# Optimization experiments

Measured on AMD Instinct MI355X. Metric: run time of the kernel, lower is better.

## Reference

```python
import jax, jax.numpy as jnp
import numpy as np

N_WAY = 5
K_SHOT = 1
QUERY = 75          # queries per class -> 375 total
PRJ = 14            # projections per support class
C, H, W = 512, 10, 10
NUM_NODE = H * W
SINK_EPS = 0.05     # entropic regularization (on max-normalized cost)
SINK_ITERS = 50


def setup_inputs() -> dict:
    key = jax.random.key(0)
    k1, k2 = jax.random.split(key)
    n_support = N_WAY * K_SHOT * PRJ
    num_query = N_WAY * QUERY
    feat = jax.random.normal(k1, (n_support + num_query, C, H, W), dtype=jnp.float32)
    label = jax.random.randint(k2, (num_query,), 0, N_WAY)
    return {"feat": feat, "label": label}


def _sinkhorn(cost, r, c, eps=SINK_EPS, iters=SINK_ITERS):
    """Batched entropic OT (log-domain Sinkhorn), replacing the per-pair
    cv2.EMD CPU solve. cost: [..., n, m]; r: [..., n]; c: [..., m].
    r and c each sum to NUM_NODE, so total transported mass is NUM_NODE,
    matching the cv2.EMD flow scale. Scaling the cost by a positive scalar
    does not change the (exact-)OT plan, so we max-normalize per pair for a
    consistent effective regularization."""
    scale = jnp.max(cost, axis=(-1, -2), keepdims=True) + 1e-6
    cost = cost / scale
    log_r = jnp.log(r)
    log_c = jnp.log(c)

    def body(fg, _):
        f, g = fg
        f = eps * (log_r - jax.nn.logsumexp((g[..., None, :] - cost) / eps, axis=-1))
        g = eps * (log_c - jax.nn.logsumexp((f[..., :, None] - cost) / eps, axis=-2))
        return (f, g), None

    init = (jnp.zeros_like(r), jnp.zeros_like(c))
    (f, g), _ = jax.lax.scan(body, init, None, length=iters)
    return jnp.exp((f[..., :, None] + g[..., None, :] - cost) / eps)


def reference(feat, label):
    n_support = N_WAY * K_SHOT * PRJ
    support = feat[:n_support].reshape(N_WAY, PRJ, C, H, W)
    query = feat[n_support:]                       # [nq, C, H, W]
    proto = support.mean(axis=1)                   # [way, C, H, W]
    nq = query.shape[0]

    # --- get_weight_vector: <A_node_feat, global_avg(B)> per (A,B) pair ---
    proto_avg = proto.mean(axis=(2, 3))            # [way, C]
    query_avg = query.mean(axis=(2, 3))            # [nq, C]
    qf = query.reshape(nq, C, NUM_NODE)
    pf = proto.reshape(N_WAY, C, NUM_NODE)
    w1 = jax.nn.relu(jnp.einsum('mcp,nc->mnp', qf, proto_avg)) + 0.001  # [nq, way, N]
    w2 = jax.nn.relu(jnp.einsum('ncp,mc->nmp', pf, query_avg)) + 0.001  # [way, nq, N]

    # --- normalize_feature: subtract channel mean ---
    protoN = proto - proto.mean(axis=1, keepdims=True)
    queryN = query - query.mean(axis=1, keepdims=True)

    # --- similarity map: 1 - squared L2 over channels, per node pair ---
    p = protoN.reshape(N_WAY, C, NUM_NODE).transpose(0, 2, 1)  # [way, N, C]
    q = queryN.reshape(nq, C, NUM_NODE).transpose(0, 2, 1)     # [nq, N, C]
    qn = (q ** 2).sum(-1)                                      # [nq, N]
    pn = (p ** 2).sum(-1)                                      # [way, N]
    cross = jnp.einsum('iac,jbc->ijab', q, p)                  # [nq, way, N, N]
    sqd = qn[:, None, :, None] + pn[None, :, None, :] - 2.0 * cross
    sim = 1.0 - sqd                                            # similarity_map
    cost = sqd                                                 # = 1 - sim

    # --- marginal weights, normalized to sum NUM_NODE (as in emd_inference) ---
    ww1 = jax.nn.relu(w1) + 1e-5
    ww1 = ww1 * (NUM_NODE / ww1.sum(-1, keepdims=True))        # [nq, way, N]
    ww2 = jax.nn.relu(jnp.transpose(w2, (1, 0, 2))) + 1e-5     # weight_2[j,i] -> [nq, way, N]
    ww2 = ww2 * (NUM_NODE / ww2.sum(-1, keepdims=True))

    # --- OT flow (detached, like torch.from_numpy(flow)) ---
    flow = jax.lax.stop_gradient(
        _sinkhorn(jax.lax.stop_gradient(cost), jax.lax.stop_gradient(ww1), jax.lax.stop_gradient(ww2))
    )

    temperature = 12.5 / NUM_NODE
    logits = (sim * flow).sum((-1, -2)) * temperature          # [nq, way]
    log_p_y = jax.nn.log_softmax(logits, axis=1)
    loss = -jnp.take_along_axis(log_p_y, label[:, None], axis=1).mean()
    return (log_p_y, loss)
```

## Files before the change

### kernel.cpp

```cpp
#include <hip/hip_runtime.h>
#include <math.h>

#define NW   5
#define PRJ  14
#define CCH  512
#define PP   100
#define NQ   375
#define NS   70
#define NPAIR (NQ*NW)

#define OFF_PROTO   0
#define OFF_PAVG    256000
#define OFF_QAVG    258560
#define OFF_QSQ     450560
#define OFF_PSQ     488060
#define OFF_LOGITS  488560
#define OFF_PF16    490440
#define OFF_AUX     654280
#define OFF_KG      1036780
#define REQ_WS_BYTES ((size_t)(OFF_KG + 18750000 + 64) * 4)

typedef float f32x16 __attribute__((ext_vector_type(16)));
typedef _Float16 f16x2 __attribute__((ext_vector_type(2)));
typedef _Float16 f16x8 __attribute__((ext_vector_type(8)));

__device__ __forceinline__ int SWZ(int n) { return n ^ ((n >> 2) & 7); }

__global__ void k_proto(const float* __restrict__ feat, float* __restrict__ ws) {
    int nc = blockIdx.x;
    int n  = nc >> 9;
    int p  = threadIdx.x;
    float s = 0.f;
    if (p < PP) {
        const float* base = feat + (size_t)((n * PRJ) * CCH) * PP + (size_t)(nc & 511) * PP + p;
        #pragma unroll
        for (int k = 0; k < PRJ; ++k) s += base[(size_t)k * CCH * PP];
        s *= (1.f / PRJ);
        ws[OFF_PROTO + nc * PP + p] = s;
    }
    float v = (p < PP) ? s : 0.f;
    #pragma unroll
    for (int off = 32; off; off >>= 1) v += __shfl_down(v, off);
    __shared__ float red[2];
    if ((threadIdx.x & 63) == 0) red[threadIdx.x >> 6] = v;
    __syncthreads();
    if (threadIdx.x == 0) ws[OFF_PAVG + nc] = (red[0] + red[1]) * (1.f / PP);
}

__global__ __launch_bounds__(256) void k_qstat(const float* __restrict__ src,
                                               float* __restrict__ dst_sq,
                                               float* __restrict__ dst_avg) {
    __shared__ __align__(16) float t[6400];
    int b = blockIdx.x, tid = threadIdx.x;
    const float* base = src + (size_t)b * CCH * PP;
    float qsq = 0.f;
    for (int c0 = 0; c0 < CCH; c0 += 64) {
        __syncthreads();
        const float4* g = (const float4*)(base + (size_t)c0 * PP);
        for (int i = tid; i < 1600; i += 256) ((float4*)t)[i] = g[i];
        __syncthreads();
        if (tid < PP) {
            #pragma unroll 8
            for (int c = 0; c < 64; ++c) { float x = t[c * PP + tid]; qsq = fmaf(x, x, qsq); }
        } else if (tid >= 128 && tid < 192) {
            int ch = tid - 128;
            const float4* row = (const float4*)(t + ch * PP);
            float s = 0.f;
            #pragma unroll
            for (int i = 0; i < 25; ++i) { float4 v = row[i]; s += (v.x + v.y) + (v.z + v.w); }
            if (dst_avg) dst_avg[(size_t)b * CCH + c0 + ch] = s * (1.f / PP);
        }
    }
    if (tid < PP) dst_sq[b * PP + tid] = qsq;
}

__global__ __launch_bounds__(256) void k_pconv(float* __restrict__ ws) {
    int b = blockIdx.x;
    int n = b >> 4, kt = b & 15;
    int tid = threadIdx.x;
    int c0 = kt * 32;
    uint* img = (uint*)(ws + OFF_PF16) + (size_t)b * 2048;
    const float* pb = ws + OFF_PROTO + (size_t)n * CCH * PP;
    const float* pavg = ws + OFF_PAVG + n * CCH;
    for (int i = tid; i < 1600; i += 256) {
        int cp = i / 100, col = i - cp * 100;
        float a0 = pb[(size_t)(c0 + 2 * cp) * PP + col];
        float a1 = pb[(size_t)(c0 + 2 * cp + 1) * PP + col];
        uint pk = __builtin_bit_cast(uint, __builtin_amdgcn_cvt_pkrtz(a0, a1));
        img[(((cp >> 2) << 7) | SWZ(col)) * 4 + (cp & 3)] = pk;
    }
    if (tid < 16) {
        int cp = tid;
        float a0 = pavg[c0 + 2 * cp], a1 = pavg[c0 + 2 * cp + 1];
        uint pk = __builtin_bit_cast(uint, __builtin_amdgcn_cvt_pkrtz(a0, a1));
        img[(((cp >> 2) << 7) | 101) * 4 + (cp & 3)] = pk;
    }
    for (int i = tid; i < 448; i += 256) {
        int dw = i & 3; int t2 = i >> 2;
        int s_i = t2 % 28; int k4 = t2 / 28;
        int s = 100 + s_i;
        if (s == 101) continue;
        img[(((k4) << 7) | s) * 4 + dw] = (s == 100) ? 0x3C003C00u : 0u;
    }
}


__global__ __launch_bounds__(256, 4) void k_cost(const float* __restrict__ query,
                                                 float* __restrict__ ws) {
    __shared__ __align__(16) char SH[22400];
    __shared__ float wrL[PP], wcL[PP], qnl[PP], pnl[PP], sqv[PP], spv[PP];
    __shared__ float red[8];
    uint* Kst = (uint*)SH;

    int p_ = blockIdx.x;
    int xcd = p_ & 7, off_ = p_ >> 3;
    int pair = (xcd < 3) ? (xcd * 235 + off_) : (705 + (xcd - 3) * 234 + off_);

    int m = pair / NW;
    int n = pair - m * NW;
    int tid = threadIdx.x;
    int lane = tid & 63, wid = tid >> 6;
    int lrow = lane & 31, lhi = lane >> 5;

    const float* qb = query + (size_t)m * CCH * PP;
    const float* qavg_g = ws + OFF_QAVG + (size_t)m * CCH;
    const uint* pimg = (const uint*)(ws + OFF_PF16) + (size_t)n * 16 * 2048;

    for (int idx = tid; idx < 112; idx += 256) {
        int s_i = idx % 28; int k4 = idx / 28;
        int s = 100 + s_i;
        if (s == 101) continue;
        uint4 val = (s == 100)
                  ? make_uint4(0x3C003C00u, 0x3C003C00u, 0x3C003C00u, 0x3C003C00u)
                  : make_uint4(0u, 0u, 0u, 0u);
        *(uint4*)&SH[(k4 * 128 + s) * 16] = val;
    }

    f32x16 acc[4];
    #pragma unroll
    for (int tc = 0; tc < 4; ++tc)
        #pragma unroll
        for (int e = 0; e < 16; ++e) acc[tc][e] = 0.f;

    int arow16 = SWZ(32 * wid + lrow) * 16;
    int bcol16[4];
    #pragma unroll
    for (int tc = 0; tc < 4; ++tc) bcol16[tc] = SWZ(32 * tc + lrow) * 16;

    for (int kt = 0; kt < 16; ++kt) {
        int c0 = kt * 32;
        for (int idx = tid; idx < 400; idx += 256) {
            int cp = idx / 25, n4 = idx - cp * 25;
            const float* src = qb + (size_t)(c0 + 2 * cp) * PP + n4 * 4;
            float4 x0 = *(const float4*)src;
            float4 x1 = *(const float4*)(src + PP);
            const float* p0 = (const float*)&x0;
            const float* p1 = (const float*)&x1;
            int basedw = ((cp >> 2) << 7);
            int dwb = (cp & 3) * 4;
            #pragma unroll
            for (int i4 = 0; i4 < 4; ++i4) {
                int node = n4 * 4 + i4;
                uint pk = __builtin_bit_cast(uint, __builtin_amdgcn_cvt_pkrtz(p0[i4], p1[i4]));
                *(uint*)&SH[(basedw + SWZ(node)) * 16 + dwb] = pk;
            }
        }
        if (tid < 16) {
            int cp = tid;
            uint pk = __builtin_bit_cast(uint,
                __builtin_amdgcn_cvt_pkrtz(qavg_g[c0 + 2 * cp], qavg_g[c0 + 2 * cp + 1]));
            *(uint*)&SH[(((cp >> 2) << 7) + 101) * 16 + (cp & 3) * 4] = pk;
        }
        {
            const float4* gB = (const float4*)(pimg + (size_t)kt * 2048);
            float4* sB = (float4*)&SH[8192];
            for (int i = tid; i < 512; i += 256) sB[i] = gB[i];
        }
        __syncthreads();
        __builtin_amdgcn_s_setprio(1);
        #pragma unroll
        for (int s = 0; s < 2; ++s) {
            int kb = (2 * s + lhi) * 2048;
            f16x8 ah = *(const f16x8*)&SH[kb + arow16];
            #pragma unroll
            for (int tc = 0; tc < 4; ++tc) {
                f16x8 bh = *(const f16x8*)&SH[8192 + kb + bcol16[tc]];
                acc[tc] = __builtin_amdgcn_mfma_f32_32x32x16_f16(ah, bh, acc[tc], 0, 0, 0);
            }
        }
        __builtin_amdgcn_s_setprio(0);
        __syncthreads();
    }

    if ((lane & 31) == 4 || (lane & 31) == 5) {
        float* dst = ((lane & 31) == 4) ? wrL : sqv;
        #pragma unroll
        for (int reg = 0; reg < 16; ++reg) {
            int row = 32 * wid + (reg & 3) + 8 * (reg >> 2) + 4 * lhi;
            if (row < PP) dst[row] = acc[3][reg];
        }
    }
    if (wid == 3 && lhi == 1) {
        #pragma unroll
        for (int tc = 0; tc < 4; ++tc) {
            int col = 32 * tc + lrow;
            if (col < PP) { wcL[col] = acc[tc][0]; spv[col] = acc[tc][1]; }
        }
    }
    __syncthreads();

    float v1 = 0.f, v2 = 0.f;
    if (tid < PP) {
        v1 = fmaxf(wrL[tid], 0.f) + 0.00101f;
        v2 = fmaxf(wcL[tid], 0.f) + 0.00101f;
    }
    float s1 = v1, s2 = v2;
    #pragma unroll
    for (int off = 32; off; off >>= 1) { s1 += __shfl_down(s1, off); s2 += __shfl_down(s2, off); }
    if ((tid & 63) == 0) { red[tid >> 6] = s1; red[4 + (tid >> 6)] = s2; }
    __syncthreads();
    float t1 = red[0] + red[1], t2 = red[4] + red[5];
    if (tid < PP) {
        wrL[tid] = v1 * (100.f / t1) * 4.f;
        wcL[tid] = v2 * (100.f / t2) * 4.f;
        float sq = sqv[tid], sp = spv[tid];
        qnl[tid] = ws[OFF_QSQ + m * PP + tid] - sq * sq * (1.f / 512.f);
        pnl[tid] = ws[OFF_PSQ + n * PP + tid] - sp * sp * (1.f / 512.f);
    }
    __syncthreads();

    float spc[4], pnc[4];
    #pragma unroll
    for (int tc = 0; tc < 4; ++tc) {
        int col = 32 * tc + lrow;
        bool cv = col < PP;
        spc[tc] = cv ? spv[col] : 0.f;
        pnc[tc] = cv ? pnl[col] : 0.f;
    }
    float mymax = -1e30f;
    #pragma unroll
    for (int reg = 0; reg < 16; ++reg) {
        int row = 32 * wid + (reg & 3) + 8 * (reg >> 2) + 4 * lhi;
        bool rv = row < PP;
        float sqr = rv ? sqv[row] : 0.f;
        float qnr = rv ? qnl[row] : 0.f;
        #pragma unroll
        for (int tc = 0; tc < 4; ++tc) {
            float sqd = qnr + pnc[tc] - 2.f * (acc[tc][reg] - sqr * spc[tc] * (1.f / 512.f));
            acc[tc][reg] = sqd;
            int col = 32 * tc + lrow;
            if (rv && col < PP) mymax = fmaxf(mymax, sqd);
        }
    }
    #pragma unroll
    for (int off = 32; off; off >>= 1) mymax = fmaxf(mymax, __shfl_down(mymax, off));
    __syncthreads();
    if (lane == 0) red[wid] = mymax;
    __syncthreads();
    float scale = fmaxf(fmaxf(red[0], red[1]), fmaxf(red[2], red[3])) + 1e-6f;
    float k2 = (1.f / scale) * (20.f * 1.44269504088896f);

    #pragma unroll
    for (int tc = 0; tc < 4; ++tc) {
        float kv[16];
        #pragma unroll
        for (int reg = 0; reg < 16; ++reg) kv[reg] = exp2f(fmaf(-acc[tc][reg], k2, 15.f));
        int col = 32 * tc + lrow;
        #pragma unroll
        for (int reg = 0; reg < 16; ++reg) {
            float pv = __shfl_xor(kv[reg], 1);
            int row = 32 * wid + (reg & 3) + 8 * (reg >> 2) + 4 * lhi;
            if (!(lane & 1) && row < PP && col < PP) {
                int j = col >> 1;
                int dw = (j < 25) ? j : (j + 3);
                uint pk = __builtin_bit_cast(uint, __builtin_amdgcn_cvt_pkrtz(kv[reg], pv));
                Kst[row * 56 + dw] = pk;
            }
        }
    }
    __syncthreads();

    int r_ = tid >> 1, hf = tid & 1;
    bool sact = tid < 200;
    if (sact) {
        uint Kr[25], KTr[25];
        const uint* rp = Kst + r_ * 56 + 28 * hf;
        #pragma unroll
        for (int q = 0; q < 25; ++q) Kr[q] = rp[q];
        int j = r_ >> 1;
        int dwc = (j < 25) ? j : (j + 3);
        int sh = (r_ & 1) * 16;
        const uint* cp0 = Kst + (50 * hf) * 56 + dwc;
        #pragma unroll
        for (int q = 0; q < 25; ++q) {
            uint d0 = cp0[(2 * q) * 56];
            uint d1 = cp0[(2 * q + 1) * 56];
            KTr[q] = ((d0 >> sh) & 0xFFFFu) | (((d1 >> sh) & 0xFFFFu) << 16);
        }
        uint* kg = (uint*)(ws + OFF_KG) + (size_t)pair * 10000 + (r_ >> 1);
        int ibR = (r_ & 1) * 50 + 25 * hf;
        int ibT = 100 + (r_ & 1) * 50 + 25 * hf;
        #pragma unroll
        for (int q = 0; q < 25; ++q) kg[(ibR + q) * 50] = Kr[q];
        #pragma unroll
        for (int q = 0; q < 25; ++q) kg[(ibT + q) * 50] = KTr[q];
    }
    float* aux = ws + OFF_AUX + (size_t)pair * 204;
    if (tid < PP) { aux[tid] = wrL[tid]; aux[100 + tid] = wcL[tid]; }
    if (tid == 0) aux[200] = scale;
}

__global__ __launch_bounds__(64, 2) void k_sink(float* __restrict__ ws) {
    __shared__ __align__(16) uint uhL[52], vhL[52];
    int pair = blockIdx.x;
    int l = threadIdx.x;
    bool act = l < 50;

    const float* aux = ws + OFF_AUX + (size_t)pair * 204;
    float wr0 = 0.f, wr1 = 0.f, wc0 = 0.f, wc1 = 0.f;
    if (act) {
        wr0 = aux[2 * l]; wr1 = aux[2 * l + 1];
        wc0 = aux[100 + 2 * l]; wc1 = aux[101 + 2 * l];
    }
    float scale = aux[200];
    float rk2 = scale * (1.f / (20.f * 1.44269504088896f));

    uint K0[50], K1[50], T0[50], T1[50];
    {
        const uint* kg = (const uint*)(ws + OFF_KG) + (size_t)pair * 10000 + (l < 50 ? l : 0);
        #pragma unroll
        for (int i = 0; i < 50; ++i) K0[i] = kg[i * 50];
        #pragma unroll
        for (int i = 0; i < 50; ++i) K1[i] = kg[(50 + i) * 50];
        #pragma unroll
        for (int i = 0; i < 50; ++i) T0[i] = kg[(100 + i) * 50];
        #pragma unroll
        for (int i = 0; i < 50; ++i) T1[i] = kg[(150 + i) * 50];
    }
    if (l < 52) { vhL[l] = (l < 50) ? 0x3C003C00u : 0u; uhL[l] = 0u; }
    __syncthreads();

    float u0 = 0.f, u1 = 0.f;
    for (int it = 0; it < 50; ++it) {
        if (act) {
            const uint4* vp4 = (const uint4*)vhL;
            float a0 = 0.f, b0 = 0.f, a1 = 0.f, b1 = 0.f;
            #pragma unroll
            for (int d4 = 0; d4 < 12; ++d4) {
                uint4 V = vp4[d4];
                a0 = __builtin_amdgcn_fdot2(__builtin_bit_cast(f16x2, K0[4*d4+0]), __builtin_bit_cast(f16x2, V.x), a0, false);
                b0 = __builtin_amdgcn_fdot2(__builtin_bit_cast(f16x2, K0[4*d4+1]), __builtin_bit_cast(f16x2, V.y), b0, false);
                a0 = __builtin_amdgcn_fdot2(__builtin_bit_cast(f16x2, K0[4*d4+2]), __builtin_bit_cast(f16x2, V.z), a0, false);
                b0 = __builtin_amdgcn_fdot2(__builtin_bit_cast(f16x2, K0[4*d4+3]), __builtin_bit_cast(f16x2, V.w), b0, false);
                a1 = __builtin_amdgcn_fdot2(__builtin_bit_cast(f16x2, K1[4*d4+0]), __builtin_bit_cast(f16x2, V.x), a1, false);
                b1 = __builtin_amdgcn_fdot2(__builtin_bit_cast(f16x2, K1[4*d4+1]), __builtin_bit_cast(f16x2, V.y), b1, false);
                a1 = __builtin_amdgcn_fdot2(__builtin_bit_cast(f16x2, K1[4*d4+2]), __builtin_bit_cast(f16x2, V.z), a1, false);
                b1 = __builtin_amdgcn_fdot2(__builtin_bit_cast(f16x2, K1[4*d4+3]), __builtin_bit_cast(f16x2, V.w), b1, false);
            }
            {
                uint v48 = vhL[48], v49 = vhL[49];
                a0 = __builtin_amdgcn_fdot2(__builtin_bit_cast(f16x2, K0[48]), __builtin_bit_cast(f16x2, v48), a0, false);
                b0 = __builtin_amdgcn_fdot2(__builtin_bit_cast(f16x2, K0[49]), __builtin_bit_cast(f16x2, v49), b0, false);
                a1 = __builtin_amdgcn_fdot2(__builtin_bit_cast(f16x2, K1[48]), __builtin_bit_cast(f16x2, v48), a1, false);
                b1 = __builtin_amdgcn_fdot2(__builtin_bit_cast(f16x2, K1[49]), __builtin_bit_cast(f16x2, v49), b1, false);
            }
            u0 = fminf(wr0 * __builtin_amdgcn_rcpf(a0 + b0), 60000.f);
            u1 = fminf(wr1 * __builtin_amdgcn_rcpf(a1 + b1), 60000.f);
            uhL[l] = __builtin_bit_cast(uint, __builtin_amdgcn_cvt_pkrtz(u0, u1));
        }
        __syncthreads();
        if (act) {
            const uint4* up4 = (const uint4*)uhL;
            float a0 = 0.f, b0 = 0.f, a1 = 0.f, b1 = 0.f;
            #pragma unroll
            for (int d4 = 0; d4 < 12; ++d4) {
                uint4 U = up4[d4];
                a0 = __builtin_amdgcn_fdot2(__builtin_bit_cast(f16x2, T0[4*d4+0]), __builtin_bit_cast(f16x2, U.x), a0, false);
                b0 = __builtin_amdgcn_fdot2(__builtin_bit_cast(f16x2, T0[4*d4+1]), __builtin_bit_cast(f16x2, U.y), b0, false);
                a0 = __builtin_amdgcn_fdot2(__builtin_bit_cast(f16x2, T0[4*d4+2]), __builtin_bit_cast(f16x2, U.z), a0, false);
                b0 = __builtin_amdgcn_fdot2(__builtin_bit_cast(f16x2, T0[4*d4+3]), __builtin_bit_cast(f16x2, U.w), b0, false);
                a1 = __builtin_amdgcn_fdot2(__builtin_bit_cast(f16x2, T1[4*d4+0]), __builtin_bit_cast(f16x2, U.x), a1, false);
                b1 = __builtin_amdgcn_fdot2(__builtin_bit_cast(f16x2, T1[4*d4+1]), __builtin_bit_cast(f16x2, U.y), b1, false);
                a1 = __builtin_amdgcn_fdot2(__builtin_bit_cast(f16x2, T1[4*d4+2]), __builtin_bit_cast(f16x2, U.z), a1, false);
                b1 = __builtin_amdgcn_fdot2(__builtin_bit_cast(f16x2, T1[4*d4+3]), __builtin_bit_cast(f16x2, U.w), b1, false);
            }
            {
                uint u48 = uhL[48], u49 = uhL[49];
                a0 = __builtin_amdgcn_fdot2(__builtin_bit_cast(f16x2, T0[48]), __builtin_bit_cast(f16x2, u48), a0, false);
                b0 = __builtin_amdgcn_fdot2(__builtin_bit_cast(f16x2, T0[49]), __builtin_bit_cast(f16x2, u49), b0, false);
                a1 = __builtin_amdgcn_fdot2(__builtin_bit_cast(f16x2, T1[48]), __builtin_bit_cast(f16x2, u48), a1, false);
                b1 = __builtin_amdgcn_fdot2(__builtin_bit_cast(f16x2, T1[49]), __builtin_bit_cast(f16x2, u49), b1, false);
            }
            float v0 = fminf(wc0 * __builtin_amdgcn_rcpf(a0 + b0), 60000.f);
            float v1n = fminf(wc1 * __builtin_amdgcn_rcpf(a1 + b1), 60000.f);
            vhL[l] = __builtin_bit_cast(uint, __builtin_amdgcn_cvt_pkrtz(v0, v1n));
        }
        __syncthreads();
    }

    float lsum = 0.f;
    if (act) {
        float l0 = 0.f, l1 = 0.f;
        #pragma unroll
        for (int d = 0; d < 50; ++d) {
            f16x2 vv = __builtin_bit_cast(f16x2, vhL[d]);
            f16x2 h0 = __builtin_bit_cast(f16x2, K0[d]);
            f16x2 h1 = __builtin_bit_cast(f16x2, K1[d]);
            float k00 = (float)h0[0], k01 = (float)h0[1];
            float k10 = (float)h1[0], k11 = (float)h1[1];
            float v0 = (float)vv[0], v1v = (float)vv[1];
            l0 = fmaf((1.f - (15.f - __log2f(k00)) * rk2) * k00, v0, l0);
            l0 = fmaf((1.f - (15.f - __log2f(k01)) * rk2) * k01, v1v, l0);
            l1 = fmaf((1.f - (15.f - __log2f(k10)) * rk2) * k10, v0, l1);
            l1 = fmaf((1.f - (15.f - __log2f(k11)) * rk2) * k11, v1v, l1);
        }
        lsum = l0 * u0 + l1 * u1;
    }
    #pragma unroll
    for (int off = 32; off; off >>= 1) lsum += __shfl_down(lsum, off);
    if (l == 0) ws[OFF_LOGITS + pair] = lsum * (0.125f / 4.f);
}

__global__ __launch_bounds__(256, 4) void k_pair(const float* __restrict__ query,
                                                 float* __restrict__ ws) {
    __shared__ __align__(16) char SH[22400];
    __shared__ __align__(16) uint uh[56], vh[56];
    __shared__ float wrL[PP], wcL[PP], qnl[PP], pnl[PP], sqv[PP], spv[PP];
    __shared__ float red[8];
    uint* Kst = (uint*)SH;

    int p_ = blockIdx.x;
    int xcd = p_ & 7, off_ = p_ >> 3;
    int pair = (xcd < 3) ? (xcd * 235 + off_) : (705 + (xcd - 3) * 234 + off_);

    int m = pair / NW;
    int n = pair - m * NW;
    int tid = threadIdx.x;
    int lane = tid & 63, wid = tid >> 6;
    int lrow = lane & 31, lhi = lane >> 5;

    const float* qb = query + (size_t)m * CCH * PP;
    const float* qavg_g = ws + OFF_QAVG + (size_t)m * CCH;
    const uint* pimg = (const uint*)(ws + OFF_PF16) + (size_t)n * 16 * 2048;

    for (int idx = tid; idx < 112; idx += 256) {
        int s_i = idx % 28; int k4 = idx / 28;
        int s = 100 + s_i;
        if (s == 101) continue;
        uint4 val = (s == 100)
                  ? make_uint4(0x3C003C00u, 0x3C003C00u, 0x3C003C00u, 0x3C003C00u)
                  : make_uint4(0u, 0u, 0u, 0u);
        *(uint4*)&SH[(k4 * 128 + s) * 16] = val;
    }

    f32x16 acc[4];
    #pragma unroll
    for (int tc = 0; tc < 4; ++tc)
        #pragma unroll
        for (int e = 0; e < 16; ++e) acc[tc][e] = 0.f;

    int arow16 = SWZ(32 * wid + lrow) * 16;
    int bcol16[4];
    #pragma unroll
    for (int tc = 0; tc < 4; ++tc) bcol16[tc] = SWZ(32 * tc + lrow) * 16;

    for (int kt = 0; kt < 16; ++kt) {
        int c0 = kt * 32;
        for (int idx = tid; idx < 400; idx += 256) {
            int cp = idx / 25, n4 = idx - cp * 25;
            const float* src = qb + (size_t)(c0 + 2 * cp) * PP + n4 * 4;
            float4 x0 = *(const float4*)src;
            float4 x1 = *(const float4*)(src + PP);
            const float* p0 = (const float*)&x0;
            const float* p1 = (const float*)&x1;
            int basedw = ((cp >> 2) << 7);
            int dwb = (cp & 3) * 4;
            #pragma unroll
            for (int i4 = 0; i4 < 4; ++i4) {
                int node = n4 * 4 + i4;
                uint pk = __builtin_bit_cast(uint, __builtin_amdgcn_cvt_pkrtz(p0[i4], p1[i4]));
                *(uint*)&SH[(basedw + SWZ(node)) * 16 + dwb] = pk;
            }
        }
        if (tid < 16) {
            int cp = tid;
            uint pk = __builtin_bit_cast(uint,
                __builtin_amdgcn_cvt_pkrtz(qavg_g[c0 + 2 * cp], qavg_g[c0 + 2 * cp + 1]));
            *(uint*)&SH[(((cp >> 2) << 7) + 101) * 16 + (cp & 3) * 4] = pk;
        }
        {
            const float4* gB = (const float4*)(pimg + (size_t)kt * 2048);
            float4* sB = (float4*)&SH[8192];
            for (int i = tid; i < 512; i += 256) sB[i] = gB[i];
        }
        __syncthreads();
        __builtin_amdgcn_s_setprio(1);
        #pragma unroll
        for (int s = 0; s < 2; ++s) {
            int kb = (2 * s + lhi) * 2048;
            f16x8 ah = *(const f16x8*)&SH[kb + arow16];
            #pragma unroll
            for (int tc = 0; tc < 4; ++tc) {
                f16x8 bh = *(const f16x8*)&SH[8192 + kb + bcol16[tc]];
                acc[tc] = __builtin_amdgcn_mfma_f32_32x32x16_f16(ah, bh, acc[tc], 0, 0, 0);
            }
        }
        __builtin_amdgcn_s_setprio(0);
        __syncthreads();
    }

    if ((lane & 31) == 4 || (lane & 31) == 5) {
        float* dst = ((lane & 31) == 4) ? wrL : sqv;
        #pragma unroll
        for (int reg = 0; reg < 16; ++reg) {
            int row = 32 * wid + (reg & 3) + 8 * (reg >> 2) + 4 * lhi;
            if (row < PP) dst[row] = acc[3][reg];
        }
    }
    if (wid == 3 && lhi == 1) {
        #pragma unroll
        for (int tc = 0; tc < 4; ++tc) {
            int col = 32 * tc + lrow;
            if (col < PP) { wcL[col] = acc[tc][0]; spv[col] = acc[tc][1]; }
        }
    }
    if (tid < 56) {
        vh[tid] = (tid < 25 || (tid >= 28 && tid < 53)) ? 0x3C003C00u : 0u;
        uh[tid] = 0u;
    }
    __syncthreads();

    float v1 = 0.f, v2 = 0.f;
    if (tid < PP) {
        v1 = fmaxf(wrL[tid], 0.f) + 0.00101f;
        v2 = fmaxf(wcL[tid], 0.f) + 0.00101f;
    }
    float s1 = v1, s2 = v2;
    #pragma unroll
    for (int off = 32; off; off >>= 1) { s1 += __shfl_down(s1, off); s2 += __shfl_down(s2, off); }
    if ((tid & 63) == 0) { red[tid >> 6] = s1; red[4 + (tid >> 6)] = s2; }
    __syncthreads();
    float t1 = red[0] + red[1], t2 = red[4] + red[5];
    if (tid < PP) {
        wrL[tid] = v1 * (100.f / t1) * 4.f;
        wcL[tid] = v2 * (100.f / t2) * 4.f;
        float sq = sqv[tid], sp = spv[tid];
        qnl[tid] = ws[OFF_QSQ + m * PP + tid] - sq * sq * (1.f / 512.f);
        pnl[tid] = ws[OFF_PSQ + n * PP + tid] - sp * sp * (1.f / 512.f);
    }
    __syncthreads();

    float spc[4], pnc[4];
    #pragma unroll
    for (int tc = 0; tc < 4; ++tc) {
        int col = 32 * tc + lrow;
        bool cv = col < PP;
        spc[tc] = cv ? spv[col] : 0.f;
        pnc[tc] = cv ? pnl[col] : 0.f;
    }
    float mymax = -1e30f;
    #pragma unroll
    for (int reg = 0; reg < 16; ++reg) {
        int row = 32 * wid + (reg & 3) + 8 * (reg >> 2) + 4 * lhi;
        bool rv = row < PP;
        float sqr = rv ? sqv[row] : 0.f;
        float qnr = rv ? qnl[row] : 0.f;
        #pragma unroll
        for (int tc = 0; tc < 4; ++tc) {
            float sqd = qnr + pnc[tc] - 2.f * (acc[tc][reg] - sqr * spc[tc] * (1.f / 512.f));
            acc[tc][reg] = sqd;
            int col = 32 * tc + lrow;
            if (rv && col < PP) mymax = fmaxf(mymax, sqd);
        }
    }
    #pragma unroll
    for (int off = 32; off; off >>= 1) mymax = fmaxf(mymax, __shfl_down(mymax, off));
    __syncthreads();
    if (lane == 0) red[wid] = mymax;
    __syncthreads();
    float scale = fmaxf(fmaxf(red[0], red[1]), fmaxf(red[2], red[3])) + 1e-6f;
    float k2 = (1.f / scale) * (20.f * 1.44269504088896f);

    #pragma unroll
    for (int tc = 0; tc < 4; ++tc) {
        float kv[16];
        #pragma unroll
        for (int reg = 0; reg < 16; ++reg) kv[reg] = exp2f(fmaf(-acc[tc][reg], k2, 15.f));
        int col = 32 * tc + lrow;
        #pragma unroll
        for (int reg = 0; reg < 16; ++reg) {
            float pv = __shfl_xor(kv[reg], 1);
            int row = 32 * wid + (reg & 3) + 8 * (reg >> 2) + 4 * lhi;
            if (!(lane & 1) && row < PP && col < PP) {
                int j = col >> 1;
                int dw = (j < 25) ? j : (j + 3);
                uint pk = __builtin_bit_cast(uint, __builtin_amdgcn_cvt_pkrtz(kv[reg], pv));
                Kst[row * 56 + dw] = pk;
            }
        }
    }
    __syncthreads();

    int r_ = tid >> 1, hf = tid & 1;
    bool sact = tid < 200;
    uint Kr[25], KTr[25];
    float wr_own = 0.f, wc_own = 0.f;
    if (sact) {
        const uint* rp = Kst + r_ * 56 + 28 * hf;
        #pragma unroll
        for (int q = 0; q < 25; ++q) Kr[q] = rp[q];
        int j = r_ >> 1;
        int dwc = (j < 25) ? j : (j + 3);
        int sh = (r_ & 1) * 16;
        const uint* cp0 = Kst + (50 * hf) * 56 + dwc;
        #pragma unroll
        for (int q = 0; q < 25; ++q) {
            uint d0 = cp0[(2 * q) * 56];
            uint d1 = cp0[(2 * q + 1) * 56];
            KTr[q] = ((d0 >> sh) & 0xFFFFu) | (((d1 >> sh) & 0xFFFFu) << 16);
        }
        wr_own = wrL[r_];
        wc_own = wcL[r_];
    }
    __syncthreads();

    int tpk = tid >> 2;
    float u_ = 0.f, v_ = 0.f;
    for (int it = 0; it < 50; ++it) {
        if (sact) {
            uint4 vv[7];
            const uint4* vp4 = (const uint4*)(vh + hf * 28);
            #pragma unroll
            for (int i = 0; i < 7; ++i) vv[i] = vp4[i];
            const uint* vw = (const uint*)vv;
            float s = 0.f;
            #pragma unroll
            for (int q = 0; q < 25; ++q)
                s = __builtin_amdgcn_fdot2(__builtin_bit_cast(f16x2, Kr[q]),
                                           __builtin_bit_cast(f16x2, vw[q]), s, false);
            s += __shfl_xor(s, 1);
            u_ = fminf(wr_own * __builtin_amdgcn_rcpf(s), 60000.f);
        }
        {
            float u_nb = __shfl_down(u_, 2);
            if (sact && (tid & 3) == 0)
                uh[tpk + (tpk >= 25 ? 3 : 0)] =
                    __builtin_bit_cast(uint, __builtin_amdgcn_cvt_pkrtz(u_, u_nb));
        }
        __syncthreads();
        if (sact) {
            uint4 uu[7];
            const uint4* up4 = (const uint4*)(uh + hf * 28);
            #pragma unroll
            for (int i = 0; i < 7; ++i) uu[i] = up4[i];
            const uint* uw = (const uint*)uu;
            float s = 0.f;
            #pragma unroll
            for (int q = 0; q < 25; ++q)
                s = __builtin_amdgcn_fdot2(__builtin_bit_cast(f16x2, KTr[q]),
                                           __builtin_bit_cast(f16x2, uw[q]), s, false);
            s += __shfl_xor(s, 1);
            v_ = fminf(wc_own * __builtin_amdgcn_rcpf(s), 60000.f);
        }
        {
            float v_nb = __shfl_down(v_, 2);
            if (sact && (tid & 3) == 0)
                vh[tpk + (tpk >= 25 ? 3 : 0)] =
                    __builtin_bit_cast(uint, __builtin_amdgcn_cvt_pkrtz(v_, v_nb));
        }
        __syncthreads();
    }

    float lsum = 0.f;
    if (sact) {
        const uint* vp = vh + hf * 28;
        float rk2 = scale * (1.f / (20.f * 1.44269504088896f));
        #pragma unroll
        for (int q = 0; q < 25; ++q) {
            f16x2 h = __builtin_bit_cast(f16x2, Kr[q]);
            f16x2 vv = __builtin_bit_cast(f16x2, vp[q]);
            float k0 = (float)h[0], k1 = (float)h[1];
            float sq0 = (15.f - __log2f(k0)) * rk2;
            float sq1 = (15.f - __log2f(k1)) * rk2;
            lsum = fmaf((1.f - sq0) * k0, (float)vv[0], lsum);
            lsum = fmaf((1.f - sq1) * k1, (float)vv[1], lsum);
        }
        lsum *= u_;
    }
    #pragma unroll
    for (int off = 32; off; off >>= 1) lsum += __shfl_down(lsum, off);
    if (lane == 0) red[wid] = lsum;
    __syncthreads();
    if (tid == 0)
        ws[OFF_LOGITS + pair] = ((red[0] + red[1]) + (red[2] + red[3])) * (0.125f / 4.f);
}

__global__ void k_final(const int* __restrict__ label, const float* __restrict__ ws,
                        float* __restrict__ out) {
    int t = threadIdx.x;
    float contrib = 0.f;
    if (t < NQ) {
        float lg[NW];
        #pragma unroll
        for (int n = 0; n < NW; ++n) lg[n] = ws[OFF_LOGITS + t * NW + n];
        float mx = lg[0];
        #pragma unroll
        for (int n = 1; n < NW; ++n) mx = fmaxf(mx, lg[n]);
        float s = 0.f;
        #pragma unroll
        for (int n = 0; n < NW; ++n) s += expf(lg[n] - mx);
        float lse = mx + logf(s);
        int lab = label[t];
        #pragma unroll
        for (int n = 0; n < NW; ++n) {
            float lp = lg[n] - lse;
            out[t * NW + n] = lp;
            if (n == lab) contrib = -lp;
        }
    }
    #pragma unroll
    for (int off = 32; off; off >>= 1) contrib += __shfl_down(contrib, off);
    __shared__ float red[6];
    if ((t & 63) == 0) red[t >> 6] = contrib;
    __syncthreads();
    if (t == 0) {
        float s = 0.f;
        #pragma unroll
        for (int i = 0; i < 6; ++i) s += red[i];
        out[NQ * NW] = s * (1.f / NQ);
    }
}

extern "C" void kernel_launch(void* const* d_in, const int* in_sizes, int n_in,
                              void* d_out, int out_size, void* d_ws, size_t ws_size,
                              hipStream_t stream) {
    const float* feat  = (const float*)d_in[0];
    const int*   label = (const int*)d_in[1];
    float* out = (float*)d_out;
    float* ws  = (float*)d_ws;
    const float* query = feat + (size_t)NS * CCH * PP;

    k_proto<<<NW * CCH, 128, 0, stream>>>(feat, ws);
    k_qstat<<<NQ, 256, 0, stream>>>(query, ws + OFF_QSQ, ws + OFF_QAVG);
    k_qstat<<<NW, 256, 0, stream>>>(ws + OFF_PROTO, ws + OFF_PSQ, (float*)nullptr);
    k_pconv<<<NW * 16, 256, 0, stream>>>(ws);
    if (ws_size >= REQ_WS_BYTES) {
        k_cost<<<NPAIR, 256, 0, stream>>>(query, ws);
        k_sink<<<NPAIR, 64, 0, stream>>>(ws);
    } else {
        k_pair<<<NPAIR, 256, 0, stream>>>(query, ws);
    }
    k_final<<<1, 384, 0, stream>>>(label, ws, out);
}
```

Baseline: 226.8 us.

## Pre-convert query features to fp16 swizzled images once, reuse across class pairs

```diff
diff --git a/kernel.cpp b/kernel.cpp
--- a/kernel.cpp
+++ b/kernel.cpp
@@ -18,7 +18,9 @@
 #define OFF_PF16    490440
 #define OFF_AUX     654280
 #define OFF_KG      1036780
-#define REQ_WS_BYTES ((size_t)(OFF_KG + 18750000 + 64) * 4)
+#define OFF_QF16    19786844
+#define REQ1_WS_BYTES ((size_t)(OFF_KG + 18750000 + 64) * 4)
+#define REQ2_WS_BYTES ((size_t)(OFF_QF16 + 12288000 + 64) * 4)
 
 typedef float f32x16 __attribute__((ext_vector_type(16)));
 typedef _Float16 f16x2 __attribute__((ext_vector_type(2)));
@@ -74,14 +76,16 @@
     if (tid < PP) dst_sq[b * PP + tid] = qsq;
 }
 
-__global__ __launch_bounds__(256) void k_pconv(float* __restrict__ ws) {
+__global__ __launch_bounds__(256) void k_conv(const float* __restrict__ src,
+                                              const float* __restrict__ avg,
+                                              uint* __restrict__ dst) {
     int b = blockIdx.x;
-    int n = b >> 4, kt = b & 15;
+    int id = b >> 4, kt = b & 15;
     int tid = threadIdx.x;
     int c0 = kt * 32;
-    uint* img = (uint*)(ws + OFF_PF16) + (size_t)b * 2048;
-    const float* pb = ws + OFF_PROTO + (size_t)n * CCH * PP;
-    const float* pavg = ws + OFF_PAVG + n * CCH;
+    uint* img = dst + (size_t)b * 2048;
+    const float* pb = src + (size_t)id * CCH * PP;
+    const float* pavg = avg + (size_t)id * CCH;
     for (int i = tid; i < 1600; i += 256) {
         int cp = i / 100, col = i - cp * 100;
         float a0 = pb[(size_t)(c0 + 2 * cp) * PP + col];
@@ -105,8 +109,175 @@
 }
 
 
-__global__ __launch_bounds__(256, 4) void k_cost(const float* __restrict__ query,
-                                                 float* __restrict__ ws) {
+__global__ __launch_bounds__(256, 4) void k_cost2(float* __restrict__ ws) {
+    __shared__ __align__(16) char SH[22400];
+    __shared__ float wrL[PP], wcL[PP], qnl[PP], pnl[PP], sqv[PP], spv[PP];
+    __shared__ float red[8];
+    uint* Kst = (uint*)SH;
+
+    int p_ = blockIdx.x;
+    int xcd = p_ & 7, off_ = p_ >> 3;
+    int pair = (xcd < 3) ? (xcd * 235 + off_) : (705 + (xcd - 3) * 234 + off_);
+
+    int m = pair / NW;
+    int n = pair - m * NW;
+    int tid = threadIdx.x;
+    int lane = tid & 63, wid = tid >> 6;
+    int lrow = lane & 31, lhi = lane >> 5;
+
+    const char* qimg = (const char*)((const uint*)(ws + OFF_QF16) + (size_t)m * 16 * 2048);
+    const char* pimg = (const char*)((const uint*)(ws + OFF_PF16) + (size_t)n * 16 * 2048);
+
+    f32x16 acc[4];
+    #pragma unroll
+    for (int tc = 0; tc < 4; ++tc)
+        #pragma unroll
+        for (int e = 0; e < 16; ++e) acc[tc][e] = 0.f;
+
+    int arow16 = SWZ(32 * wid + lrow) * 16;
+    int bcol16[4];
+    #pragma unroll
+    for (int tc = 0; tc < 4; ++tc) bcol16[tc] = SWZ(32 * tc + lrow) * 16;
+
+    #pragma unroll 2
+    for (int kt = 0; kt < 16; ++kt) {
+        const char* qk = qimg + kt * 8192;
+        const char* pk = pimg + kt * 8192;
+        #pragma unroll
+        for (int s = 0; s < 2; ++s) {
+            int kb = (2 * s + lhi) * 2048;
+            f16x8 ah = *(const f16x8*)(qk + kb + arow16);
+            f16x8 b0 = *(const f16x8*)(pk + kb + bcol16[0]);
+            f16x8 b1 = *(const f16x8*)(pk + kb + bcol16[1]);
+            f16x8 b2 = *(const f16x8*)(pk + kb + bcol16[2]);
+            f16x8 b3 = *(const f16x8*)(pk + kb + bcol16[3]);
+            acc[0] = __builtin_amdgcn_mfma_f32_32x32x16_f16(ah, b0, acc[0], 0, 0, 0);
+            acc[1] = __builtin_amdgcn_mfma_f32_32x32x16_f16(ah, b1, acc[1], 0, 0, 0);
+            acc[2] = __builtin_amdgcn_mfma_f32_32x32x16_f16(ah, b2, acc[2], 0, 0, 0);
+            acc[3] = __builtin_amdgcn_mfma_f32_32x32x16_f16(ah, b3, acc[3], 0, 0, 0);
+        }
+    }
+
+    if ((lane & 31) == 4 || (lane & 31) == 5) {
+        float* dst = ((lane & 31) == 4) ? wrL : sqv;
+        #pragma unroll
+        for (int reg = 0; reg < 16; ++reg) {
+            int row = 32 * wid + (reg & 3) + 8 * (reg >> 2) + 4 * lhi;
+            if (row < PP) dst[row] = acc[3][reg];
+        }
+    }
+    if (wid == 3 && lhi == 1) {
+        #pragma unroll
+        for (int tc = 0; tc < 4; ++tc) {
+            int col = 32 * tc + lrow;
+            if (col < PP) { wcL[col] = acc[tc][0]; spv[col] = acc[tc][1]; }
+        }
+    }
+    __syncthreads();
+
+    float v1 = 0.f, v2 = 0.f;
+    if (tid < PP) {
+        v1 = fmaxf(wrL[tid], 0.f) + 0.00101f;
+        v2 = fmaxf(wcL[tid], 0.f) + 0.00101f;
+    }
+    float s1 = v1, s2 = v2;
+    #pragma unroll
+    for (int off = 32; off; off >>= 1) { s1 += __shfl_down(s1, off); s2 += __shfl_down(s2, off); }
+    if ((tid & 63) == 0) { red[tid >> 6] = s1; red[4 + (tid >> 6)] = s2; }
+    __syncthreads();
+    float t1 = red[0] + red[1], t2 = red[4] + red[5];
+    if (tid < PP) {
+        wrL[tid] = v1 * (100.f / t1) * 4.f;
+        wcL[tid] = v2 * (100.f / t2) * 4.f;
+        float sq = sqv[tid], sp = spv[tid];
+        qnl[tid] = ws[OFF_QSQ + m * PP + tid] - sq * sq * (1.f / 512.f);
+        pnl[tid] = ws[OFF_PSQ + n * PP + tid] - sp * sp * (1.f / 512.f);
+    }
+    __syncthreads();
+
+    float spc[4], pnc[4];
+    #pragma unroll
+    for (int tc = 0; tc < 4; ++tc) {
+        int col = 32 * tc + lrow;
+        bool cv = col < PP;
+        spc[tc] = cv ? spv[col] : 0.f;
+        pnc[tc] = cv ? pnl[col] : 0.f;
+    }
+    float mymax = -1e30f;
+    #pragma unroll
+    for (int reg = 0; reg < 16; ++reg) {
+        int row = 32 * wid + (reg & 3) + 8 * (reg >> 2) + 4 * lhi;
+        bool rv = row < PP;
+        float sqr = rv ? sqv[row] : 0.f;
+        float qnr = rv ? qnl[row] : 0.f;
+        #pragma unroll
+        for (int tc = 0; tc < 4; ++tc) {
+            float sqd = qnr + pnc[tc] - 2.f * (acc[tc][reg] - sqr * spc[tc] * (1.f / 512.f));
+            acc[tc][reg] = sqd;
+            int col = 32 * tc + lrow;
+            if (rv && col < PP) mymax = fmaxf(mymax, sqd);
+        }
+    }
+    #pragma unroll
+    for (int off = 32; off; off >>= 1) mymax = fmaxf(mymax, __shfl_down(mymax, off));
+    __syncthreads();
+    if (lane == 0) red[wid] = mymax;
+    __syncthreads();
+    float scale = fmaxf(fmaxf(red[0], red[1]), fmaxf(red[2], red[3])) + 1e-6f;
+    float k2 = (1.f / scale) * (20.f * 1.44269504088896f);
+
+    #pragma unroll
+    for (int tc = 0; tc < 4; ++tc) {
+        float kv[16];
+        #pragma unroll
+        for (int reg = 0; reg < 16; ++reg) kv[reg] = exp2f(fmaf(-acc[tc][reg], k2, 15.f));
+        int col = 32 * tc + lrow;
+        #pragma unroll
+        for (int reg = 0; reg < 16; ++reg) {
+            float pv = __shfl_xor(kv[reg], 1);
+            int row = 32 * wid + (reg & 3) + 8 * (reg >> 2) + 4 * lhi;
+            if (!(lane & 1) && row < PP && col < PP) {
+                int j = col >> 1;
+                int dw = (j < 25) ? j : (j + 3);
+                uint pk = __builtin_bit_cast(uint, __builtin_amdgcn_cvt_pkrtz(kv[reg], pv));
+                Kst[row * 56 + dw] = pk;
+            }
+        }
+    }
+    __syncthreads();
+
+    int r_ = tid >> 1, hf = tid & 1;
+    bool sact = tid < 200;
+    if (sact) {
+        uint Kr[25], KTr[25];
+        const uint* rp = Kst + r_ * 56 + 28 * hf;
+        #pragma unroll
+        for (int q = 0; q < 25; ++q) Kr[q] = rp[q];
+        int j = r_ >> 1;
+        int dwc = (j < 25) ? j : (j + 3);
+        int sh = (r_ & 1) * 16;
+        const uint* cp0 = Kst + (50 * hf) * 56 + dwc;
+        #pragma unroll
+        for (int q = 0; q < 25; ++q) {
+            uint d0 = cp0[(2 * q) * 56];
+            uint d1 = cp0[(2 * q + 1) * 56];
+            KTr[q] = ((d0 >> sh) & 0xFFFFu) | (((d1 >> sh) & 0xFFFFu) << 16);
+        }
+        uint* kg = (uint*)(ws + OFF_KG) + (size_t)pair * 10000 + (r_ >> 1);
+        int ibR = (r_ & 1) * 50 + 25 * hf;
+        int ibT = 100 + (r_ & 1) * 50 + 25 * hf;
+        #pragma unroll
+        for (int q = 0; q < 25; ++q) kg[(ibR + q) * 50] = Kr[q];
+        #pragma unroll
+        for (int q = 0; q < 25; ++q) kg[(ibT + q) * 50] = KTr[q];
+    }
+    float* aux = ws + OFF_AUX + (size_t)pair * 204;
+    if (tid < PP) { aux[tid] = wrL[tid]; aux[100 + tid] = wcL[tid]; }
+    if (tid == 0) aux[200] = scale;
+}
+
+__global__ __launch_bounds__(256, 4) void k_costL(const float* __restrict__ query,
+                                                  float* __restrict__ ws) {
     __shared__ __align__(16) char SH[22400];
     __shared__ float wrL[PP], wcL[PP], qnl[PP], pnl[PP], sqv[PP], spv[PP];
     __shared__ float red[8];
@@ -421,280 +592,6 @@
     if (l == 0) ws[OFF_LOGITS + pair] = lsum * (0.125f / 4.f);
 }
 
-__global__ __launch_bounds__(256, 4) void k_pair(const float* __restrict__ query,
-                                                 float* __restrict__ ws) {
-    __shared__ __align__(16) char SH[22400];
-    __shared__ __align__(16) uint uh[56], vh[56];
-    __shared__ float wrL[PP], wcL[PP], qnl[PP], pnl[PP], sqv[PP], spv[PP];
-    __shared__ float red[8];
-    uint* Kst = (uint*)SH;
-
-    int p_ = blockIdx.x;
-    int xcd = p_ & 7, off_ = p_ >> 3;
-    int pair = (xcd < 3) ? (xcd * 235 + off_) : (705 + (xcd - 3) * 234 + off_);
-
-    int m = pair / NW;
-    int n = pair - m * NW;
-    int tid = threadIdx.x;
-    int lane = tid & 63, wid = tid >> 6;
-    int lrow = lane & 31, lhi = lane >> 5;
-
-    const float* qb = query + (size_t)m * CCH * PP;
-    const float* qavg_g = ws + OFF_QAVG + (size_t)m * CCH;
-    const uint* pimg = (const uint*)(ws + OFF_PF16) + (size_t)n * 16 * 2048;
-
-    for (int idx = tid; idx < 112; idx += 256) {
-        int s_i = idx % 28; int k4 = idx / 28;
-        int s = 100 + s_i;
-        if (s == 101) continue;
-        uint4 val = (s == 100)
-                  ? make_uint4(0x3C003C00u, 0x3C003C00u, 0x3C003C00u, 0x3C003C00u)
-                  : make_uint4(0u, 0u, 0u, 0u);
-        *(uint4*)&SH[(k4 * 128 + s) * 16] = val;
-    }
-
-    f32x16 acc[4];
-    #pragma unroll
-    for (int tc = 0; tc < 4; ++tc)
-        #pragma unroll
-        for (int e = 0; e < 16; ++e) acc[tc][e] = 0.f;
-
-    int arow16 = SWZ(32 * wid + lrow) * 16;
-    int bcol16[4];
-    #pragma unroll
-    for (int tc = 0; tc < 4; ++tc) bcol16[tc] = SWZ(32 * tc + lrow) * 16;
-
-    for (int kt = 0; kt < 16; ++kt) {
-        int c0 = kt * 32;
-        for (int idx = tid; idx < 400; idx += 256) {
-            int cp = idx / 25, n4 = idx - cp * 25;
-            const float* src = qb + (size_t)(c0 + 2 * cp) * PP + n4 * 4;
-            float4 x0 = *(const float4*)src;
-            float4 x1 = *(const float4*)(src + PP);
-            const float* p0 = (const float*)&x0;
-            const float* p1 = (const float*)&x1;
-            int basedw = ((cp >> 2) << 7);
-            int dwb = (cp & 3) * 4;
-            #pragma unroll
-            for (int i4 = 0; i4 < 4; ++i4) {
-                int node = n4 * 4 + i4;
-                uint pk = __builtin_bit_cast(uint, __builtin_amdgcn_cvt_pkrtz(p0[i4], p1[i4]));
-                *(uint*)&SH[(basedw + SWZ(node)) * 16 + dwb] = pk;
-            }
-        }
-        if (tid < 16) {
-            int cp = tid;
-            uint pk = __builtin_bit_cast(uint,
-                __builtin_amdgcn_cvt_pkrtz(qavg_g[c0 + 2 * cp], qavg_g[c0 + 2 * cp + 1]));
-            *(uint*)&SH[(((cp >> 2) << 7) + 101) * 16 + (cp & 3) * 4] = pk;
-        }
-        {
-            const float4* gB = (const float4*)(pimg + (size_t)kt * 2048);
-            float4* sB = (float4*)&SH[8192];
-            for (int i = tid; i < 512; i += 256) sB[i] = gB[i];
-        }
-        __syncthreads();
-        __builtin_amdgcn_s_setprio(1);
-        #pragma unroll
-        for (int s = 0; s < 2; ++s) {
-            int kb = (2 * s + lhi) * 2048;
-            f16x8 ah = *(const f16x8*)&SH[kb + arow16];
-            #pragma unroll
-            for (int tc = 0; tc < 4; ++tc) {
-                f16x8 bh = *(const f16x8*)&SH[8192 + kb + bcol16[tc]];
-                acc[tc] = __builtin_amdgcn_mfma_f32_32x32x16_f16(ah, bh, acc[tc], 0, 0, 0);
-            }
-        }
-        __builtin_amdgcn_s_setprio(0);
-        __syncthreads();
-    }
-
-    if ((lane & 31) == 4 || (lane & 31) == 5) {
-        float* dst = ((lane & 31) == 4) ? wrL : sqv;
-        #pragma unroll
-        for (int reg = 0; reg < 16; ++reg) {
-            int row = 32 * wid + (reg & 3) + 8 * (reg >> 2) + 4 * lhi;
-            if (row < PP) dst[row] = acc[3][reg];
-        }
-    }
-    if (wid == 3 && lhi == 1) {
-        #pragma unroll
-        for (int tc = 0; tc < 4; ++tc) {
-            int col = 32 * tc + lrow;
-            if (col < PP) { wcL[col] = acc[tc][0]; spv[col] = acc[tc][1]; }
-        }
-    }
-    if (tid < 56) {
-        vh[tid] = (tid < 25 || (tid >= 28 && tid < 53)) ? 0x3C003C00u : 0u;
-        uh[tid] = 0u;
-    }
-    __syncthreads();
-
-    float v1 = 0.f, v2 = 0.f;
-    if (tid < PP) {
-        v1 = fmaxf(wrL[tid], 0.f) + 0.00101f;
-        v2 = fmaxf(wcL[tid], 0.f) + 0.00101f;
-    }
-    float s1 = v1, s2 = v2;
-    #pragma unroll
-    for (int off = 32; off; off >>= 1) { s1 += __shfl_down(s1, off); s2 += __shfl_down(s2, off); }
-    if ((tid & 63) == 0) { red[tid >> 6] = s1; red[4 + (tid >> 6)] = s2; }
-    __syncthreads();
-    float t1 = red[0] + red[1], t2 = red[4] + red[5];
-    if (tid < PP) {
-        wrL[tid] = v1 * (100.f / t1) * 4.f;
-        wcL[tid] = v2 * (100.f / t2) * 4.f;
-        float sq = sqv[tid], sp = spv[tid];
-        qnl[tid] = ws[OFF_QSQ + m * PP + tid] - sq * sq * (1.f / 512.f);
-        pnl[tid] = ws[OFF_PSQ + n * PP + tid] - sp * sp * (1.f / 512.f);
-    }
-    __syncthreads();
-
-    float spc[4], pnc[4];
-    #pragma unroll
-    for (int tc = 0; tc < 4; ++tc) {
-        int col = 32 * tc + lrow;
-        bool cv = col < PP;
-        spc[tc] = cv ? spv[col] : 0.f;
-        pnc[tc] = cv ? pnl[col] : 0.f;
-    }
-    float mymax = -1e30f;
-    #pragma unroll
-    for (int reg = 0; reg < 16; ++reg) {
-        int row = 32 * wid + (reg & 3) + 8 * (reg >> 2) + 4 * lhi;
-        bool rv = row < PP;
-        float sqr = rv ? sqv[row] : 0.f;
-        float qnr = rv ? qnl[row] : 0.f;
-        #pragma unroll
-        for (int tc = 0; tc < 4; ++tc) {
-            float sqd = qnr + pnc[tc] - 2.f * (acc[tc][reg] - sqr * spc[tc] * (1.f / 512.f));
-            acc[tc][reg] = sqd;
-            int col = 32 * tc + lrow;
-            if (rv && col < PP) mymax = fmaxf(mymax, sqd);
-        }
-    }
-    #pragma unroll
-    for (int off = 32; off; off >>= 1) mymax = fmaxf(mymax, __shfl_down(mymax, off));
-    __syncthreads();
-    if (lane == 0) red[wid] = mymax;
-    __syncthreads();
-    float scale = fmaxf(fmaxf(red[0], red[1]), fmaxf(red[2], red[3])) + 1e-6f;
-    float k2 = (1.f / scale) * (20.f * 1.44269504088896f);
-
-    #pragma unroll
-    for (int tc = 0; tc < 4; ++tc) {
-        float kv[16];
-        #pragma unroll
-        for (int reg = 0; reg < 16; ++reg) kv[reg] = exp2f(fmaf(-acc[tc][reg], k2, 15.f));
-        int col = 32 * tc + lrow;
-        #pragma unroll
-        for (int reg = 0; reg < 16; ++reg) {
-            float pv = __shfl_xor(kv[reg], 1);
-            int row = 32 * wid + (reg & 3) + 8 * (reg >> 2) + 4 * lhi;
-            if (!(lane & 1) && row < PP && col < PP) {
-                int j = col >> 1;
-                int dw = (j < 25) ? j : (j + 3);
-                uint pk = __builtin_bit_cast(uint, __builtin_amdgcn_cvt_pkrtz(kv[reg], pv));
-                Kst[row * 56 + dw] = pk;
-            }
-        }
-    }
-    __syncthreads();
-
-    int r_ = tid >> 1, hf = tid & 1;
-    bool sact = tid < 200;
-    uint Kr[25], KTr[25];
-    float wr_own = 0.f, wc_own = 0.f;
-    if (sact) {
-        const uint* rp = Kst + r_ * 56 + 28 * hf;
-        #pragma unroll
-        for (int q = 0; q < 25; ++q) Kr[q] = rp[q];
-        int j = r_ >> 1;
-        int dwc = (j < 25) ? j : (j + 3);
-        int sh = (r_ & 1) * 16;
-        const uint* cp0 = Kst + (50 * hf) * 56 + dwc;
-        #pragma unroll
-        for (int q = 0; q < 25; ++q) {
-            uint d0 = cp0[(2 * q) * 56];
-            uint d1 = cp0[(2 * q + 1) * 56];
-            KTr[q] = ((d0 >> sh) & 0xFFFFu) | (((d1 >> sh) & 0xFFFFu) << 16);
-        }
-        wr_own = wrL[r_];
-        wc_own = wcL[r_];
-    }
-    __syncthreads();
-
-    int tpk = tid >> 2;
-    float u_ = 0.f, v_ = 0.f;
-    for (int it = 0; it < 50; ++it) {
-        if (sact) {
-            uint4 vv[7];
-            const uint4* vp4 = (const uint4*)(vh + hf * 28);
-            #pragma unroll
-            for (int i = 0; i < 7; ++i) vv[i] = vp4[i];
-            const uint* vw = (const uint*)vv;
-            float s = 0.f;
-            #pragma unroll
-            for (int q = 0; q < 25; ++q)
-                s = __builtin_amdgcn_fdot2(__builtin_bit_cast(f16x2, Kr[q]),
-                                           __builtin_bit_cast(f16x2, vw[q]), s, false);
-            s += __shfl_xor(s, 1);
-            u_ = fminf(wr_own * __builtin_amdgcn_rcpf(s), 60000.f);
-        }
-        {
-            float u_nb = __shfl_down(u_, 2);
-            if (sact && (tid & 3) == 0)
-                uh[tpk + (tpk >= 25 ? 3 : 0)] =
-                    __builtin_bit_cast(uint, __builtin_amdgcn_cvt_pkrtz(u_, u_nb));
-        }
-        __syncthreads();
-        if (sact) {
-            uint4 uu[7];
-            const uint4* up4 = (const uint4*)(uh + hf * 28);
-            #pragma unroll
-            for (int i = 0; i < 7; ++i) uu[i] = up4[i];
-            const uint* uw = (const uint*)uu;
-            float s = 0.f;
-            #pragma unroll
-            for (int q = 0; q < 25; ++q)
-                s = __builtin_amdgcn_fdot2(__builtin_bit_cast(f16x2, KTr[q]),
-                                           __builtin_bit_cast(f16x2, uw[q]), s, false);
-            s += __shfl_xor(s, 1);
-            v_ = fminf(wc_own * __builtin_amdgcn_rcpf(s), 60000.f);
-        }
-        {
-            float v_nb = __shfl_down(v_, 2);
-            if (sact && (tid & 3) == 0)
-                vh[tpk + (tpk >= 25 ? 3 : 0)] =
-                    __builtin_bit_cast(uint, __builtin_amdgcn_cvt_pkrtz(v_, v_nb));
-        }
-        __syncthreads();
-    }
-
-    float lsum = 0.f;
-    if (sact) {
-        const uint* vp = vh + hf * 28;
-        float rk2 = scale * (1.f / (20.f * 1.44269504088896f));
-        #pragma unroll
-        for (int q = 0; q < 25; ++q) {
-            f16x2 h = __builtin_bit_cast(f16x2, Kr[q]);
-            f16x2 vv = __builtin_bit_cast(f16x2, vp[q]);
-            float k0 = (float)h[0], k1 = (float)h[1];
-            float sq0 = (15.f - __log2f(k0)) * rk2;
-            float sq1 = (15.f - __log2f(k1)) * rk2;
-            lsum = fmaf((1.f - sq0) * k0, (float)vv[0], lsum);
-            lsum = fmaf((1.f - sq1) * k1, (float)vv[1], lsum);
-        }
-        lsum *= u_;
-    }
-    #pragma unroll
-    for (int off = 32; off; off >>= 1) lsum += __shfl_down(lsum, off);
-    if (lane == 0) red[wid] = lsum;
-    __syncthreads();
-    if (tid == 0)
-        ws[OFF_LOGITS + pair] = ((red[0] + red[1]) + (red[2] + red[3])) * (0.125f / 4.f);
-}
-
 __global__ void k_final(const int* __restrict__ label, const float* __restrict__ ws,
                         float* __restrict__ out) {
     int t = threadIdx.x;
@@ -743,12 +640,14 @@
     k_proto<<<NW * CCH, 128, 0, stream>>>(feat, ws);
     k_qstat<<<NQ, 256, 0, stream>>>(query, ws + OFF_QSQ, ws + OFF_QAVG);
     k_qstat<<<NW, 256, 0, stream>>>(ws + OFF_PROTO, ws + OFF_PSQ, (float*)nullptr);
-    k_pconv<<<NW * 16, 256, 0, stream>>>(ws);
-    if (ws_size >= REQ_WS_BYTES) {
-        k_cost<<<NPAIR, 256, 0, stream>>>(query, ws);
+    k_conv<<<NW * 16, 256, 0, stream>>>(ws + OFF_PROTO, ws + OFF_PAVG, (uint*)(ws + OFF_PF16));
+    if (ws_size >= REQ2_WS_BYTES) {
+        k_conv<<<NQ * 16, 256, 0, stream>>>(query, ws + OFF_QAVG, (uint*)(ws + OFF_QF16));
+        k_cost2<<<NPAIR, 256, 0, stream>>>(ws);
         k_sink<<<NPAIR, 64, 0, stream>>>(ws);
     } else {
-        k_pair<<<NPAIR, 256, 0, stream>>>(query, ws);
+        k_costL<<<NPAIR, 256, 0, stream>>>(query, ws);
+        k_sink<<<NPAIR, 64, 0, stream>>>(ws);
     }
     k_final<<<1, 384, 0, stream>>>(label, ws, out);
 }
```

Result: slower. 232.9 us (+2.7%).
